# Kernel tuning notes

Hardware: AMD Instinct MI355X
Metric: run time of the kernel (lower is better)

## Reference

```python
import jax, jax.numpy as jnp
import numpy as np

B, N, DEG = 16, 2048, 16          # graphs, nodes per graph, avg out-degree
C_IN, HID, K = 64, 128, 32        # in_channels, hidden_channels, out_channels (clusters)
NT = B * N                        # total nodes
E = NT * DEG                      # total edges
GN_EPS = 1e-5


def setup_inputs() -> dict:
    key = jax.random.key(0)
    ks = jax.random.split(key, 6)
    x = jax.random.normal(ks[0], (NT, C_IN), jnp.float32)
    # within-graph random edges (sorted batch => node i belongs to graph i // N)
    src_l = jax.random.randint(ks[1], (E,), 0, N)
    dst_l = jax.random.randint(ks[2], (E,), 0, N)
    gid = jnp.repeat(jnp.arange(B, dtype=jnp.int32), N * DEG)
    edge_index = jnp.stack([gid * N + src_l, gid * N + dst_l]).astype(jnp.int32)
    batch = jnp.repeat(jnp.arange(B, dtype=jnp.int32), N)
    return dict(
        x=x, edge_index=edge_index, batch=batch,
        gn_weight=jnp.ones((C_IN,), jnp.float32),
        gn_bias=jnp.zeros((C_IN,), jnp.float32),
        gn_mean_scale=jnp.ones((C_IN,), jnp.float32),
        w1=jax.random.normal(ks[3], (C_IN, HID), jnp.float32) / np.float32(np.sqrt(C_IN)),
        b1=jnp.zeros((HID,), jnp.float32),
        w2=jax.random.normal(ks[4], (HID, K), jnp.float32) / np.float32(np.sqrt(HID)),
        b2=jnp.zeros((K,), jnp.float32),
    )


def reference(x, gn_weight, gn_bias, gn_mean_scale, w1, b1, w2, b2, edge_index, batch):
    # ---- GraphNorm (per-graph mean/var with learnable mean scale) ----
    ones_n = jnp.ones((NT,), x.dtype)
    cnt = jax.ops.segment_sum(ones_n, batch, num_segments=B)[:, None]        # [B,1]
    mean = jax.ops.segment_sum(x, batch, num_segments=B) / cnt              # [B,C]
    xm = x - gn_mean_scale * mean[batch]
    var = jax.ops.segment_sum(xm * xm, batch, num_segments=B) / cnt         # [B,C]
    h = gn_weight * xm / jnp.sqrt(var + GN_EPS)[batch] + gn_bias            # [NT,C_IN]

    # ---- GCNConv (add self-loops, symmetric D^-1/2 (A+I) D^-1/2) ----
    src, dst = edge_index[0], edge_index[1]
    loop = jnp.arange(NT, dtype=src.dtype)
    src_l = jnp.concatenate([src, loop])
    dst_l = jnp.concatenate([dst, loop])
    deg = jax.ops.segment_sum(jnp.ones_like(src_l, x.dtype), dst_l, num_segments=NT)
    dinv = jnp.where(deg > 0, jax.lax.rsqrt(deg), 0.0)
    norm = dinv[src_l] * dinv[dst_l]                                        # [E+NT]
    hw = h @ w1                                                             # [NT,HID]
    h = jax.ops.segment_sum(norm[:, None] * hw[src_l], dst_l, num_segments=NT) + b1
    h = jax.nn.selu(h)

    # ---- to_dense_batch / to_dense_adj (uniform graph sizes -> mask all True) ----
    xd = h.reshape(B, N, HID)                                               # [B,N,F]
    adj = jnp.zeros((B, N, N), x.dtype).at[batch[src], src % N, dst % N].add(1.0)

    # ---- DMoNPooling ----
    s = jax.nn.softmax(xd @ w2 + b2, axis=-1)                               # [B,N,K]
    out = jax.nn.selu(jnp.einsum('bnk,bnf->bkf', s, xd))                    # [B,K,F]
    sta = jnp.einsum('bnk,bnm->bkm', s, adj)                                # [B,K,N]
    out_adj = jnp.einsum('bkm,bml->bkl', sta, s)                            # [B,K,K]

    degrees = adj.sum(-1)                                                   # [B,N]
    m = degrees.sum(-1) / 2                                                 # [B]
    ca = jnp.einsum('bnk,bn->bk', s, degrees)                               # [B,K]
    normalizer = ca[:, :, None] * ca[:, None, :] / 2 / m[:, None, None]
    spectral_loss = (-jnp.einsum('bkk->b', out_adj - normalizer) / (2 * m)).mean()

    ss = jnp.einsum('bnk,bnl->bkl', s, s)                                   # [B,K,K]
    ss_fro = jnp.sqrt(jnp.sum(ss * ss, axis=(-2, -1), keepdims=True))
    eye = jnp.eye(K, dtype=x.dtype)
    diff = ss / ss_fro - eye / jnp.sqrt(jnp.float32(K))
    ortho_loss = jnp.sqrt(jnp.sum(diff * diff, axis=(-2, -1))).mean()

    cluster_size = s.sum(1)                                                 # [B,K]
    cluster_loss = (jnp.linalg.norm(cluster_size, axis=1) / N
                    * jnp.sqrt(jnp.float32(K)) - 1).mean()
    # (coarsened-adj renormalization in DMoNPooling is unused by Net's outputs)

    return jax.nn.log_softmax(out, axis=-1), spectral_loss + ortho_loss + cluster_loss, s
```

## Files before the change

### kernel.cpp

```cpp
#include <hip/hip_runtime.h>
#include <cmath>

static constexpr int B_  = 16;
static constexpr int N_  = 2048;
static constexpr int NT_ = 32768;
static constexpr int E_  = 524288;

static constexpr size_t OFF_HSC    = 0;
static constexpr size_t OFF_XD     = 2097152;
static constexpr size_t OFF_SWS    = 6291456;
static constexpr size_t OFF_PART   = 7340032;
static constexpr size_t OFF_DINV   = 9437184;
static constexpr size_t OFF_GSP    = 9469952;
static constexpr size_t OFF_GSP2   = 9478144;
static constexpr size_t OFF_SSP    = 9486336;
static constexpr size_t OFF_CAP    = 10010624;
static constexpr size_t OFF_CSP    = 10027008;
static constexpr size_t OFF_SPECP  = 10043392;
static constexpr size_t OFF_ICNTI  = 10043904;
static constexpr size_t OFF_ICNTO  = 10076672;
static constexpr size_t OFF_IROWS  = 10109440;
static constexpr size_t OFF_ICURS  = 10142212;
static constexpr size_t OFF_IESRC  = 10174980;

__device__ __forceinline__ float selu_f(float x) {
  return 1.0507009873554805f * (x > 0.f ? x : 1.6732632423543772f * expm1f(x));
}

__device__ __forceinline__ float block_sum_bcast(float v, float* sm) {
  int lane = threadIdx.x & 63, w = threadIdx.x >> 6;
#pragma unroll
  for (int off = 32; off; off >>= 1) v += __shfl_down(v, off);
  __syncthreads();
  if (lane == 0) sm[w] = v;
  __syncthreads();
  return sm[0] + sm[1] + sm[2] + sm[3];
}

__global__ __launch_bounds__(1024) void k_count(const int* ei, const float* x,
                                                int* cin, int* cout_,
                                                float* gsp, float* gsp2) {
  __shared__ int hin[2048], hout[2048];
  __shared__ float l1[16][64], l2[16][64];
  int blk = blockIdx.x;
  int tid = threadIdx.x;
  if (blk < 128) {
    int g = blk >> 3, j = blk & 7;
    int nbase = g * 2048, ebase = g * 32768 + j * 4096;
    hin[tid] = 0; hin[tid + 1024] = 0;
    hout[tid] = 0; hout[tid + 1024] = 0;
    __syncthreads();
#pragma unroll
    for (int it = 0; it < 4; it++) {
      int e = ebase + it * 1024 + tid;
      int s = ei[e], d = ei[E_ + e];
      atomicAdd(&hout[s - nbase], 1);
      atomicAdd(&hin[d - nbase], 1);
    }
    __syncthreads();
    atomicAdd(&cin[nbase + tid], hin[tid]);
    atomicAdd(&cin[nbase + tid + 1024], hin[tid + 1024]);
    atomicAdd(&cout_[nbase + tid], hout[tid]);
    atomicAdd(&cout_[nbase + tid + 1024], hout[tid + 1024]);
  } else {
    int gi = blk - 128;
    int b = gi >> 3, chunk = gi & 7;
    int c = tid & 63, r = tid >> 6;
    float s = 0.f, s2 = 0.f;
    const float* xb = x + ((size_t)b * N_ + (size_t)chunk * 256) * 64;
    for (int n = r; n < 256; n += 16) {
      float v = xb[n * 64 + c];
      s += v; s2 += v * v;
    }
    l1[r][c] = s; l2[r][c] = s2;
    __syncthreads();
    if (r == 0) {
      float t1 = 0.f, t2 = 0.f;
#pragma unroll
      for (int i = 0; i < 16; i++) { t1 += l1[i][c]; t2 += l2[i][c]; }
      gsp[gi * 64 + c] = t1;
      gsp2[gi * 64 + c] = t2;
    }
  }
}

__global__ __launch_bounds__(1024) void k_scan(const int* cin, int* rows, int* curs,
                                               float* dinv) {
  __shared__ int sb[1024];
  int g = blockIdx.x, tid = threadIdx.x;
  int nbase = g * 2048, ebase = g * 32768;
  int a = cin[nbase + 2 * tid], b2 = cin[nbase + 2 * tid + 1];
  sb[tid] = a + b2;
  __syncthreads();
  for (int off = 1; off < 1024; off <<= 1) {
    int add = (tid >= off) ? sb[tid - off] : 0;
    __syncthreads();
    sb[tid] += add;
    __syncthreads();
  }
  int pref = (tid > 0) ? sb[tid - 1] : 0;
  int r0 = ebase + pref, r1 = r0 + a;
  int n0 = nbase + 2 * tid;
  rows[n0] = r0; rows[n0 + 1] = r1;
  curs[n0] = r0; curs[n0 + 1] = r1;
  dinv[n0] = rsqrtf((float)(a + 1));
  dinv[n0 + 1] = rsqrtf((float)(b2 + 1));
  if (g == 15 && tid == 1023) rows[NT_] = E_;
}

__global__ void k_prep(const float* x, const float* gsp, const float* gsp2,
                       const float* gw, const float* gb, const float* gms,
                       const float* dinv, float* hsc,
                       const int* ei, int* curs, int* esrc) {
  __shared__ float shs[64], scs[64];
  int tid = threadIdx.x;
  int bgr = blockIdx.x >> 7;
  if (tid < 64) {
    float s = 0.f, s2 = 0.f;
#pragma unroll
    for (int c8 = 0; c8 < 8; c8++) {
      s  += gsp[(bgr * 8 + c8) * 64 + tid];
      s2 += gsp2[(bgr * 8 + c8) * 64 + tid];
    }
    float mean = s * (1.f / 2048.f);
    float a = gms[tid];
    float var = s2 * (1.f / 2048.f) - (2.f * a - a * a) * mean * mean;
    shs[tid] = a * mean;
    scs[tid] = gw[tid] * rsqrtf(var + 1e-5f);
  }
  __syncthreads();
  int idx = blockIdx.x * 256 + tid;
  int node = idx >> 4, g4 = (idx & 15) * 4;
  float di = dinv[node];
  float4 xv = *(const float4*)&x[(size_t)node * 64 + g4];
  float4 bb = *(const float4*)&gb[g4];
  float4 o;
  o.x = ((xv.x - shs[g4])     * scs[g4]     + bb.x) * di;
  o.y = ((xv.y - shs[g4 + 1]) * scs[g4 + 1] + bb.y) * di;
  o.z = ((xv.z - shs[g4 + 2]) * scs[g4 + 2] + bb.z) * di;
  o.w = ((xv.w - shs[g4 + 3]) * scs[g4 + 3] + bb.w) * di;
  *(float4*)&hsc[(size_t)node * 64 + g4] = o;
  int s = ei[idx], d = ei[E_ + idx];
  int pos = atomicAdd(&curs[d], 1);
  esrc[pos] = s;
}

__global__ __launch_bounds__(256) void k_mm1(const float* hsc, const float* dinv,
                                             const int* rows, const int* esrc,
                                             const float* w1, const float* b1,
                                             float* xd) {
  __shared__ float at[32 * 65];
  int tid = threadIdx.x;
  int n0 = blockIdx.x * 32;
  int wv = tid >> 6, c = tid & 63;
  for (int i = 0; i < 8; i++) {
    int nn = i * 4 + wv;
    int node = n0 + nn;
    int e0 = rows[node], e1 = rows[node + 1];
    float dd = dinv[node];
    float acc = hsc[(size_t)node * 64 + c];
    for (int e = e0; e < e1; e += 8) {
      int sidx[8]; float wt[8], hv[8];
#pragma unroll
      for (int j = 0; j < 8; j++) {
        int ee = e + j;
        sidx[j] = esrc[ee < e1 ? ee : e0];
        wt[j] = (ee < e1) ? 1.f : 0.f;
      }
#pragma unroll
      for (int j = 0; j < 8; j++) hv[j] = hsc[(size_t)sidx[j] * 64 + c];
#pragma unroll
      for (int j = 0; j < 8; j++) acc += wt[j] * hv[j];
    }
    at[nn * 65 + c] = dd * acc;
  }
  __syncthreads();
  int tx = tid & 31, ty = tid >> 5;
  int f0 = tx * 4, nn = ty * 4;
  float acc[4][4] = {};
  for (int k = 0; k < 64; k++) {
    float4 wvv = *(const float4*)&w1[k * 128 + f0];
#pragma unroll
    for (int i = 0; i < 4; i++) {
      float av = at[(nn + i) * 65 + k];
      acc[i][0] += av * wvv.x; acc[i][1] += av * wvv.y;
      acc[i][2] += av * wvv.z; acc[i][3] += av * wvv.w;
    }
  }
  float4 bv = *(const float4*)&b1[f0];
#pragma unroll
  for (int i = 0; i < 4; i++) {
    float4 o;
    o.x = selu_f(acc[i][0] + bv.x);
    o.y = selu_f(acc[i][1] + bv.y);
    o.z = selu_f(acc[i][2] + bv.z);
    o.w = selu_f(acc[i][3] + bv.w);
    *(float4*)&xd[(size_t)(n0 + nn + i) * 128 + f0] = o;
  }
}

__global__ __launch_bounds__(256) void k_mm2f(const float* xd, const float* w2,
                                              const float* b2, const int* cout_,
                                              float* s_ws, float* outs, float* ssp,
                                              float* cap, float* csp, float* part) {
  __shared__ float xt[64 * 129];
  __shared__ float w2s[128 * 32];
  __shared__ float st[64 * 33];
  __shared__ float r1[8][32], r2[8][32];
  int tid = threadIdx.x;
  int blk = blockIdx.x;
  int n0 = blk * 64;
  for (int i = tid; i < 4096; i += 256) w2s[i] = w2[i];
  for (int i = tid; i < 2048; i += 256) {
    int n = i >> 5, j4 = (i & 31) * 4;
    float4 v = *(const float4*)&xd[(size_t)(n0 + n) * 128 + j4];
    xt[n * 129 + j4] = v.x; xt[n * 129 + j4 + 1] = v.y;
    xt[n * 129 + j4 + 2] = v.z; xt[n * 129 + j4 + 3] = v.w;
  }
  __syncthreads();
  int ty = tid >> 3;
  int k0 = (tid & 7) * 4;
  float acc2[2][4] = {};
  for (int j = 0; j < 128; j++) {
    float4 wv = *(float4*)&w2s[j * 32 + k0];
    float x0 = xt[(ty * 2) * 129 + j];
    float x1 = xt[(ty * 2 + 1) * 129 + j];
    acc2[0][0] += x0 * wv.x; acc2[0][1] += x0 * wv.y; acc2[0][2] += x0 * wv.z; acc2[0][3] += x0 * wv.w;
    acc2[1][0] += x1 * wv.x; acc2[1][1] += x1 * wv.y; acc2[1][2] += x1 * wv.z; acc2[1][3] += x1 * wv.w;
  }
  float4 bv2 = *(const float4*)&b2[k0];
#pragma unroll
  for (int i = 0; i < 2; i++) {
    int n = ty * 2 + i;
    st[n * 33 + k0]     = acc2[i][0] + bv2.x;
    st[n * 33 + k0 + 1] = acc2[i][1] + bv2.y;
    st[n * 33 + k0 + 2] = acc2[i][2] + bv2.z;
    st[n * 33 + k0 + 3] = acc2[i][3] + bv2.w;
  }
  __syncthreads();
  if (tid < 64) {
    float m = -3.4e38f;
    for (int kk = 0; kk < 32; kk++) m = fmaxf(m, st[tid * 33 + kk]);
    float ssum = 0.f;
    for (int kk = 0; kk < 32; kk++) {
      float e = expf(st[tid * 33 + kk] - m);
      st[tid * 33 + kk] = e; ssum += e;
    }
    float inv = 1.f / ssum;
    for (int kk = 0; kk < 32; kk++) st[tid * 33 + kk] *= inv;
  }
  __syncthreads();
  for (int i = tid; i < 512; i += 256) {
    int n = i >> 3, q = (i & 7) * 4;
    float4 o = {st[n * 33 + q], st[n * 33 + q + 1], st[n * 33 + q + 2], st[n * 33 + q + 3]};
    *(float4*)&s_ws[(size_t)(n0 + n) * 32 + q] = o;
    float* op = &outs[(size_t)(n0 + n) * 32 + q];
    op[0] = o.x; op[1] = o.y; op[2] = o.z; op[3] = o.w;
  }
  {
    int k = tid >> 3, l0 = (tid & 7) * 4;
    float a0 = 0, a1 = 0, a2 = 0, a3 = 0;
    for (int n = 0; n < 64; n++) {
      float sk = st[n * 33 + k];
      a0 += sk * st[n * 33 + l0];     a1 += sk * st[n * 33 + l0 + 1];
      a2 += sk * st[n * 33 + l0 + 2]; a3 += sk * st[n * 33 + l0 + 3];
    }
    float4 o = {a0, a1, a2, a3};
    *(float4*)&ssp[(size_t)blk * 1024 + k * 32 + l0] = o;
  }
  {
    int k2 = tid & 31, r = tid >> 5;
    float aca = 0.f, acs = 0.f;
    for (int i = 0; i < 8; i++) {
      int n = i * 8 + r;
      float dg = (float)cout_[n0 + n];
      float v = st[n * 33 + k2];
      acs += v; aca += v * dg;
    }
    r1[r][k2] = aca; r2[r][k2] = acs;
    __syncthreads();
    if (r == 0) {
      float sa = 0.f, sc = 0.f;
#pragma unroll
      for (int i = 0; i < 8; i++) { sa += r1[i][k2]; sc += r2[i][k2]; }
      cap[blk * 32 + k2] = sa;
      csp[blk * 32 + k2] = sc;
    }
  }
  {
    int tx = tid & 31, ty2 = tid >> 5;
    int f0 = tx * 4, kk0 = ty2 * 4;
    float acc[4][4] = {};
    for (int n = 0; n < 64; n++) {
      float s0 = st[n * 33 + kk0], s1 = st[n * 33 + kk0 + 1];
      float s2 = st[n * 33 + kk0 + 2], s3 = st[n * 33 + kk0 + 3];
      float4 xv = {xt[n * 129 + f0], xt[n * 129 + f0 + 1], xt[n * 129 + f0 + 2], xt[n * 129 + f0 + 3]};
      acc[0][0] += s0 * xv.x; acc[0][1] += s0 * xv.y; acc[0][2] += s0 * xv.z; acc[0][3] += s0 * xv.w;
      acc[1][0] += s1 * xv.x; acc[1][1] += s1 * xv.y; acc[1][2] += s1 * xv.z; acc[1][3] += s1 * xv.w;
      acc[2][0] += s2 * xv.x; acc[2][1] += s2 * xv.y; acc[2][2] += s2 * xv.z; acc[2][3] += s2 * xv.w;
      acc[3][0] += s3 * xv.x; acc[3][1] += s3 * xv.y; acc[3][2] += s3 * xv.z; acc[3][3] += s3 * xv.w;
    }
#pragma unroll
    for (int i = 0; i < 4; i++) {
      float4 o = {acc[i][0], acc[i][1], acc[i][2], acc[i][3]};
      *(float4*)&part[(size_t)(blk * 32 + kk0 + i) * 128 + f0] = o;
    }
  }
}

__global__ __launch_bounds__(256) void k_spec(const int* ei, const float* s_ws,
                                              float* specp, float* lossp) {
  __shared__ float sm4[4];
  int blk = blockIdx.x, tid = threadIdx.x;
  if (blk == 0 && tid == 0) lossp[0] = 0.f;
  int ebase = blk * 1024;
  float acc = 0.f;
#pragma unroll
  for (int j = 0; j < 4; j++) {
    int e = ebase + j * 256 + tid;
    int s = ei[e], d = ei[E_ + e];
    const float4* ap = (const float4*)&s_ws[(size_t)s * 32];
    const float4* cp = (const float4*)&s_ws[(size_t)d * 32];
#pragma unroll
    for (int q = 0; q < 8; q++) {
      float4 u = ap[q], v = cp[q];
      acc += u.x * v.x + u.y * v.y + u.z * v.z + u.w * v.w;
    }
  }
  int lane = tid & 63, w = tid >> 6;
#pragma unroll
  for (int off = 32; off; off >>= 1) acc += __shfl_down(acc, off);
  if (lane == 0) sm4[w] = acc;
  __syncthreads();
  if (tid == 0) specp[blk] = sm4[0] + sm4[1] + sm4[2] + sm4[3];
}

__global__ void k_outf(const float* part, float* out0) {
  int row = blockIdx.x;
  int b = row >> 5, k = row & 31;
  int f = threadIdx.x;
  float v = 0.f;
#pragma unroll
  for (int c = 0; c < 32; c++) v += part[(size_t)((b * 32 + c) * 32 + k) * 128 + f];
  v = selu_f(v);
  int lane = threadIdx.x & 63, w = threadIdx.x >> 6;
  __shared__ float s1[2], s2[2];
  float m = v;
#pragma unroll
  for (int off = 32; off; off >>= 1) m = fmaxf(m, __shfl_down(m, off));
  if (lane == 0) s1[w] = m;
  __syncthreads();
  m = fmaxf(s1[0], s1[1]);
  float e = expf(v - m), t = e;
#pragma unroll
  for (int off = 32; off; off >>= 1) t += __shfl_down(t, off);
  if (lane == 0) s2[w] = t;
  __syncthreads();
  float tot = s2[0] + s2[1];
  out0[(size_t)row * 128 + f] = v - m - logf(tot);
}

__global__ void k_loss(const float* ssp, const float* csp, const float* cap,
                       const float* specp, float* loss) {
  int b = blockIdx.x;
  __shared__ float sm[4];
  int tid = threadIdx.x;
  float v0 = 0, v1 = 0, v2 = 0, v3 = 0;
  for (int c = 0; c < 32; c++) {
    float4 u = *(const float4*)&ssp[(size_t)(b * 32 + c) * 1024 + tid * 4];
    v0 += u.x; v1 += u.y; v2 += u.z; v3 += u.w;
  }
  float ssq = v0 * v0 + v1 * v1 + v2 * v2 + v3 * v3;
  ssq = block_sum_bcast(ssq, sm);
  float inv = 1.f / sqrtf(ssq);
  float dsq = 0.f;
  {
    int i0 = tid * 4;
    float vv[4] = {v0, v1, v2, v3};
#pragma unroll
    for (int j = 0; j < 4; j++) {
      int i = i0 + j;
      float d = vv[j] * inv;
      if ((i >> 5) == (i & 31)) d -= 0.17677669529663687f;
      dsq += d * d;
    }
  }
  dsq = block_sum_bcast(dsq, sm);
  float csq = 0.f, casq = 0.f;
  if (tid < 32) {
    float c1 = 0.f, c2 = 0.f;
    for (int c = 0; c < 32; c++) {
      c1 += csp[(size_t)(b * 32 + c) * 32 + tid];
      c2 += cap[(size_t)(b * 32 + c) * 32 + tid];
    }
    csq = c1 * c1; casq = c2 * c2;
  }
  csq = block_sum_bcast(csq, sm);
  casq = block_sum_bcast(casq, sm);
  float spec_sum = (tid < 32) ? specp[b * 32 + tid] : 0.f;
  spec_sum = block_sum_bcast(spec_sum, sm);
  if (tid == 0) {
    float ortho = sqrtf(dsq);
    float cl = sqrtf(csq) * (1.f / 2048.f) * 5.656854249492381f - 1.f;
    float m = 16384.f;
    float spec = -(spec_sum - casq / (2.f * m)) / (2.f * m);
    atomicAdd(loss, (spec + ortho + cl) * (1.f / 16.f));
  }
}

extern "C" void kernel_launch(void* const* d_in, const int* in_sizes, int n_in,
                              void* d_out, int out_size, void* d_ws, size_t ws_size,
                              hipStream_t stream) {
  (void)in_sizes; (void)n_in; (void)out_size; (void)ws_size;
  const float* x   = (const float*)d_in[0];
  const int*   ei  = (const int*)d_in[1];
  const float* gw  = (const float*)d_in[3];
  const float* gb  = (const float*)d_in[4];
  const float* gms = (const float*)d_in[5];
  const float* w1  = (const float*)d_in[6];
  const float* b1  = (const float*)d_in[7];
  const float* w2  = (const float*)d_in[8];
  const float* b2  = (const float*)d_in[9];
  float* out = (float*)d_out;
  float* ws  = (float*)d_ws;

  float* hsc    = ws + OFF_HSC;
  float* xd     = ws + OFF_XD;
  float* s_ws   = ws + OFF_SWS;
  float* part   = ws + OFF_PART;
  float* dinv   = ws + OFF_DINV;
  float* gsp    = ws + OFF_GSP;
  float* gsp2   = ws + OFF_GSP2;
  float* ssp    = ws + OFF_SSP;
  float* cap    = ws + OFF_CAP;
  float* csp    = ws + OFF_CSP;
  float* specp  = ws + OFF_SPECP;
  int*   cin    = (int*)(ws + OFF_ICNTI);
  int*   cout_  = (int*)(ws + OFF_ICNTO);
  int*   rows   = (int*)(ws + OFF_IROWS);
  int*   curs   = (int*)(ws + OFF_ICURS);
  int*   esrc   = (int*)(ws + OFF_IESRC);

  float* out0  = out;
  float* lossp = out + 65536;
  float* outs  = out + 65537;

  hipMemsetAsync((void*)cin, 0, 2 * NT_ * sizeof(int), stream);
  hipLaunchKernelGGL(k_count, dim3(256), dim3(1024), 0, stream, ei, x, cin, cout_, gsp, gsp2);
  hipLaunchKernelGGL(k_scan, dim3(16), dim3(1024), 0, stream, cin, rows, curs, dinv);
  hipLaunchKernelGGL(k_prep, dim3(2048), dim3(256), 0, stream,
                     x, gsp, gsp2, gw, gb, gms, dinv, hsc, ei, curs, esrc);
  hipLaunchKernelGGL(k_mm1, dim3(1024), dim3(256), 0, stream, hsc, dinv, rows, esrc, w1, b1, xd);
  hipLaunchKernelGGL(k_mm2f, dim3(512), dim3(256), 0, stream,
                     xd, w2, b2, cout_, s_ws, outs, ssp, cap, csp, part);
  hipLaunchKernelGGL(k_spec, dim3(512), dim3(256), 0, stream, ei, s_ws, specp, lossp);
  hipLaunchKernelGGL(k_outf, dim3(512), dim3(128), 0, stream, part, out0);
  hipLaunchKernelGGL(k_loss, dim3(16), dim3(256), 0, stream, ssp, csp, cap, specp, lossp);
}
```

Measured before the change: 208.0 us.

## Replace CSR build with per-block destination-filtered shared-memory aggregation; merge final kernels

Removes the prefix-scan kernel and the global-atomic bucketing of edges into CSR order. Each block instead streams all edges of its graph, uses a wave ballot to pick the edges whose destination falls in its 128-node slice, and accumulates neighbour features into shared memory with atomics before the W1 matmul. Degree normalisation is now computed on the fly from the in-degree counts. The log-softmax output kernel and the loss kernel are also merged into one launch. The cost is that every graph's edge list is read 16 times and the gather becomes a serial loop over matched lanes.

```diff
diff --git a/kernel.cpp b/kernel.cpp
--- a/kernel.cpp
+++ b/kernel.cpp
@@ -10,18 +10,14 @@
 static constexpr size_t OFF_XD     = 2097152;
 static constexpr size_t OFF_SWS    = 6291456;
 static constexpr size_t OFF_PART   = 7340032;
-static constexpr size_t OFF_DINV   = 9437184;
-static constexpr size_t OFF_GSP    = 9469952;
-static constexpr size_t OFF_GSP2   = 9478144;
-static constexpr size_t OFF_SSP    = 9486336;
-static constexpr size_t OFF_CAP    = 10010624;
-static constexpr size_t OFF_CSP    = 10027008;
-static constexpr size_t OFF_SPECP  = 10043392;
-static constexpr size_t OFF_ICNTI  = 10043904;
-static constexpr size_t OFF_ICNTO  = 10076672;
-static constexpr size_t OFF_IROWS  = 10109440;
-static constexpr size_t OFF_ICURS  = 10142212;
-static constexpr size_t OFF_IESRC  = 10174980;
+static constexpr size_t OFF_GSP    = 9437184;
+static constexpr size_t OFF_GSP2   = 9445376;
+static constexpr size_t OFF_SSP    = 9453568;
+static constexpr size_t OFF_CAP    = 9977856;
+static constexpr size_t OFF_CSP    = 9994240;
+static constexpr size_t OFF_SPECP  = 10010624;
+static constexpr size_t OFF_ICNTI  = 10011136;
+static constexpr size_t OFF_ICNTO  = 10043904;
 
 __device__ __forceinline__ float selu_f(float x) {
   return 1.0507009873554805f * (x > 0.f ? x : 1.6732632423543772f * expm1f(x));
@@ -84,34 +80,9 @@
   }
 }
 
-__global__ __launch_bounds__(1024) void k_scan(const int* cin, int* rows, int* curs,
-                                               float* dinv) {
-  __shared__ int sb[1024];
-  int g = blockIdx.x, tid = threadIdx.x;
-  int nbase = g * 2048, ebase = g * 32768;
-  int a = cin[nbase + 2 * tid], b2 = cin[nbase + 2 * tid + 1];
-  sb[tid] = a + b2;
-  __syncthreads();
-  for (int off = 1; off < 1024; off <<= 1) {
-    int add = (tid >= off) ? sb[tid - off] : 0;
-    __syncthreads();
-    sb[tid] += add;
-    __syncthreads();
-  }
-  int pref = (tid > 0) ? sb[tid - 1] : 0;
-  int r0 = ebase + pref, r1 = r0 + a;
-  int n0 = nbase + 2 * tid;
-  rows[n0] = r0; rows[n0 + 1] = r1;
-  curs[n0] = r0; curs[n0 + 1] = r1;
-  dinv[n0] = rsqrtf((float)(a + 1));
-  dinv[n0 + 1] = rsqrtf((float)(b2 + 1));
-  if (g == 15 && tid == 1023) rows[NT_] = E_;
-}
-
 __global__ void k_prep(const float* x, const float* gsp, const float* gsp2,
                        const float* gw, const float* gb, const float* gms,
-                       const float* dinv, float* hsc,
-                       const int* ei, int* curs, int* esrc) {
+                       const int* cin, float* hsc) {
   __shared__ float shs[64], scs[64];
   int tid = threadIdx.x;
   int bgr = blockIdx.x >> 7;
@@ -131,7 +102,7 @@
   __syncthreads();
   int idx = blockIdx.x * 256 + tid;
   int node = idx >> 4, g4 = (idx & 15) * 4;
-  float di = dinv[node];
+  float di = rsqrtf((float)(cin[node] + 1));
   float4 xv = *(const float4*)&x[(size_t)node * 64 + g4];
   float4 bb = *(const float4*)&gb[g4];
   float4 o;
@@ -140,62 +111,64 @@
   o.z = ((xv.z - shs[g4 + 2]) * scs[g4 + 2] + bb.z) * di;
   o.w = ((xv.w - shs[g4 + 3]) * scs[g4 + 3] + bb.w) * di;
   *(float4*)&hsc[(size_t)node * 64 + g4] = o;
-  int s = ei[idx], d = ei[E_ + idx];
-  int pos = atomicAdd(&curs[d], 1);
-  esrc[pos] = s;
-}
-
-__global__ __launch_bounds__(256) void k_mm1(const float* hsc, const float* dinv,
-                                             const int* rows, const int* esrc,
-                                             const float* w1, const float* b1,
-                                             float* xd) {
-  __shared__ float at[32 * 65];
+}
+
+__global__ __launch_bounds__(1024) void k_aggmm(const int* ei, const float* hsc,
+                                                const int* cin, const float* w1,
+                                                const float* b1, float* xd) {
+  __shared__ float acc[128 * 65];
+  int blk = blockIdx.x;
+  int g = blk >> 4, j = blk & 15;
+  int nbase = g * 2048, dstLo = j * 128;
+  int ebase = g * 32768;
   int tid = threadIdx.x;
-  int n0 = blockIdx.x * 32;
-  int wv = tid >> 6, c = tid & 63;
-  for (int i = 0; i < 8; i++) {
-    int nn = i * 4 + wv;
-    int node = n0 + nn;
-    int e0 = rows[node], e1 = rows[node + 1];
-    float dd = dinv[node];
-    float acc = hsc[(size_t)node * 64 + c];
-    for (int e = e0; e < e1; e += 8) {
-      int sidx[8]; float wt[8], hv[8];
-#pragma unroll
-      for (int j = 0; j < 8; j++) {
-        int ee = e + j;
-        sidx[j] = esrc[ee < e1 ? ee : e0];
-        wt[j] = (ee < e1) ? 1.f : 0.f;
-      }
-#pragma unroll
-      for (int j = 0; j < 8; j++) hv[j] = hsc[(size_t)sidx[j] * 64 + c];
-#pragma unroll
-      for (int j = 0; j < 8; j++) acc += wt[j] * hv[j];
-    }
-    at[nn * 65 + c] = dd * acc;
+  int wave = tid >> 6, lane = tid & 63;
+  for (int i = tid; i < 8320; i += 1024) acc[i] = 0.f;
+  __syncthreads();
+  int wbase = ebase + wave * 2048;
+  for (int it = 0; it < 32; it++) {
+    int e = wbase + it * 64 + lane;
+    int s = ei[e];
+    int d = ei[E_ + e];
+    int loc = d - nbase - dstLo;
+    unsigned long long mask = __ballot((unsigned)loc < 128u);
+    while (mask) {
+      int b = __ffsll((unsigned long long)mask) - 1;
+      mask &= mask - 1;
+      int sb = __shfl(s, b);
+      int lb = __shfl(loc, b);
+      atomicAdd(&acc[lb * 65 + lane], hsc[(size_t)sb * 64 + lane]);
+    }
+  }
+  __syncthreads();
+  for (int i = tid; i < 8192; i += 1024) {
+    int n = i >> 6, c = i & 63;
+    int node = nbase + dstLo + n;
+    float dd = rsqrtf((float)(cin[node] + 1));
+    acc[n * 65 + c] = dd * (acc[n * 65 + c] + hsc[(size_t)node * 64 + c]);
   }
   __syncthreads();
   int tx = tid & 31, ty = tid >> 5;
   int f0 = tx * 4, nn = ty * 4;
-  float acc[4][4] = {};
+  float a4[4][4] = {};
   for (int k = 0; k < 64; k++) {
-    float4 wvv = *(const float4*)&w1[k * 128 + f0];
+    float4 wv = *(const float4*)&w1[k * 128 + f0];
 #pragma unroll
     for (int i = 0; i < 4; i++) {
-      float av = at[(nn + i) * 65 + k];
-      acc[i][0] += av * wvv.x; acc[i][1] += av * wvv.y;
-      acc[i][2] += av * wvv.z; acc[i][3] += av * wvv.w;
+      float av = acc[(nn + i) * 65 + k];
+      a4[i][0] += av * wv.x; a4[i][1] += av * wv.y;
+      a4[i][2] += av * wv.z; a4[i][3] += av * wv.w;
     }
   }
   float4 bv = *(const float4*)&b1[f0];
 #pragma unroll
   for (int i = 0; i < 4; i++) {
     float4 o;
-    o.x = selu_f(acc[i][0] + bv.x);
-    o.y = selu_f(acc[i][1] + bv.y);
-    o.z = selu_f(acc[i][2] + bv.z);
-    o.w = selu_f(acc[i][3] + bv.w);
-    *(float4*)&xd[(size_t)(n0 + nn + i) * 128 + f0] = o;
+    o.x = selu_f(a4[i][0] + bv.x);
+    o.y = selu_f(a4[i][1] + bv.y);
+    o.z = selu_f(a4[i][2] + bv.z);
+    o.w = selu_f(a4[i][3] + bv.w);
+    *(float4*)&xd[(size_t)(nbase + dstLo + nn + i) * 128 + f0] = o;
   }
 }
 
@@ -335,76 +308,81 @@
   if (tid == 0) specp[blk] = sm4[0] + sm4[1] + sm4[2] + sm4[3];
 }
 
-__global__ void k_outf(const float* part, float* out0) {
-  int row = blockIdx.x;
-  int b = row >> 5, k = row & 31;
-  int f = threadIdx.x;
-  float v = 0.f;
-#pragma unroll
-  for (int c = 0; c < 32; c++) v += part[(size_t)((b * 32 + c) * 32 + k) * 128 + f];
-  v = selu_f(v);
-  int lane = threadIdx.x & 63, w = threadIdx.x >> 6;
-  __shared__ float s1[2], s2[2];
-  float m = v;
-#pragma unroll
-  for (int off = 32; off; off >>= 1) m = fmaxf(m, __shfl_down(m, off));
-  if (lane == 0) s1[w] = m;
-  __syncthreads();
-  m = fmaxf(s1[0], s1[1]);
-  float e = expf(v - m), t = e;
-#pragma unroll
-  for (int off = 32; off; off >>= 1) t += __shfl_down(t, off);
-  if (lane == 0) s2[w] = t;
-  __syncthreads();
-  float tot = s2[0] + s2[1];
-  out0[(size_t)row * 128 + f] = v - m - logf(tot);
-}
-
-__global__ void k_loss(const float* ssp, const float* csp, const float* cap,
-                       const float* specp, float* loss) {
-  int b = blockIdx.x;
-  __shared__ float sm[4];
+__global__ __launch_bounds__(256) void k_fin2(const float* part, const float* ssp,
+                                              const float* csp, const float* cap,
+                                              const float* specp, float* out0,
+                                              float* loss) {
+  __shared__ float sred[4];
+  int blk = blockIdx.x;
   int tid = threadIdx.x;
-  float v0 = 0, v1 = 0, v2 = 0, v3 = 0;
-  for (int c = 0; c < 32; c++) {
-    float4 u = *(const float4*)&ssp[(size_t)(b * 32 + c) * 1024 + tid * 4];
-    v0 += u.x; v1 += u.y; v2 += u.z; v3 += u.w;
-  }
-  float ssq = v0 * v0 + v1 * v1 + v2 * v2 + v3 * v3;
-  ssq = block_sum_bcast(ssq, sm);
-  float inv = 1.f / sqrtf(ssq);
-  float dsq = 0.f;
-  {
-    int i0 = tid * 4;
-    float vv[4] = {v0, v1, v2, v3};
-#pragma unroll
-    for (int j = 0; j < 4; j++) {
-      int i = i0 + j;
-      float d = vv[j] * inv;
-      if ((i >> 5) == (i & 31)) d -= 0.17677669529663687f;
-      dsq += d * d;
-    }
-  }
-  dsq = block_sum_bcast(dsq, sm);
-  float csq = 0.f, casq = 0.f;
-  if (tid < 32) {
-    float c1 = 0.f, c2 = 0.f;
+  if (blk < 256) {
+    int half = tid >> 7;
+    int f = tid & 127;
+    int row = blk * 2 + half;
+    int b = row >> 5, k = row & 31;
+    float v = 0.f;
+#pragma unroll
+    for (int c = 0; c < 32; c++) v += part[(size_t)((b * 32 + c) * 32 + k) * 128 + f];
+    v = selu_f(v);
+    int lane = tid & 63, w = tid >> 6;
+    float m = v;
+#pragma unroll
+    for (int off = 32; off; off >>= 1) m = fmaxf(m, __shfl_down(m, off));
+    if (lane == 0) sred[w] = m;
+    __syncthreads();
+    m = fmaxf(sred[half * 2], sred[half * 2 + 1]);
+    float e = expf(v - m);
+    float t = e;
+    __syncthreads();
+#pragma unroll
+    for (int off = 32; off; off >>= 1) t += __shfl_down(t, off);
+    if (lane == 0) sred[w] = t;
+    __syncthreads();
+    float tot = sred[half * 2] + sred[half * 2 + 1];
+    out0[(size_t)row * 128 + f] = v - m - logf(tot);
+  } else {
+    int b = blk - 256;
+    float v0 = 0, v1 = 0, v2 = 0, v3 = 0;
     for (int c = 0; c < 32; c++) {
-      c1 += csp[(size_t)(b * 32 + c) * 32 + tid];
-      c2 += cap[(size_t)(b * 32 + c) * 32 + tid];
-    }
-    csq = c1 * c1; casq = c2 * c2;
-  }
-  csq = block_sum_bcast(csq, sm);
-  casq = block_sum_bcast(casq, sm);
-  float spec_sum = (tid < 32) ? specp[b * 32 + tid] : 0.f;
-  spec_sum = block_sum_bcast(spec_sum, sm);
-  if (tid == 0) {
-    float ortho = sqrtf(dsq);
-    float cl = sqrtf(csq) * (1.f / 2048.f) * 5.656854249492381f - 1.f;
-    float m = 16384.f;
-    float spec = -(spec_sum - casq / (2.f * m)) / (2.f * m);
-    atomicAdd(loss, (spec + ortho + cl) * (1.f / 16.f));
+      float4 u = *(const float4*)&ssp[(size_t)(b * 32 + c) * 1024 + tid * 4];
+      v0 += u.x; v1 += u.y; v2 += u.z; v3 += u.w;
+    }
+    float ssq = v0 * v0 + v1 * v1 + v2 * v2 + v3 * v3;
+    ssq = block_sum_bcast(ssq, sred);
+    float inv = 1.f / sqrtf(ssq);
+    float dsq = 0.f;
+    {
+      int i0 = tid * 4;
+      float vv[4] = {v0, v1, v2, v3};
+#pragma unroll
+      for (int jj = 0; jj < 4; jj++) {
+        int i = i0 + jj;
+        float d = vv[jj] * inv;
+        if ((i >> 5) == (i & 31)) d -= 0.17677669529663687f;
+        dsq += d * d;
+      }
+    }
+    dsq = block_sum_bcast(dsq, sred);
+    float csq = 0.f, casq = 0.f;
+    if (tid < 32) {
+      float c1 = 0.f, c2 = 0.f;
+      for (int c = 0; c < 32; c++) {
+        c1 += csp[(size_t)(b * 32 + c) * 32 + tid];
+        c2 += cap[(size_t)(b * 32 + c) * 32 + tid];
+      }
+      csq = c1 * c1; casq = c2 * c2;
+    }
+    csq = block_sum_bcast(csq, sred);
+    casq = block_sum_bcast(casq, sred);
+    float spec_sum = (tid < 32) ? specp[b * 32 + tid] : 0.f;
+    spec_sum = block_sum_bcast(spec_sum, sred);
+    if (tid == 0) {
+      float ortho = sqrtf(dsq);
+      float cl = sqrtf(csq) * (1.f / 2048.f) * 5.656854249492381f - 1.f;
+      float m = 16384.f;
+      float spec = -(spec_sum - casq / (2.f * m)) / (2.f * m);
+      atomicAdd(loss, (spec + ortho + cl) * (1.f / 16.f));
+    }
   }
 }
 
@@ -428,7 +406,6 @@
   float* xd     = ws + OFF_XD;
   float* s_ws   = ws + OFF_SWS;
   float* part   = ws + OFF_PART;
-  float* dinv   = ws + OFF_DINV;
   float* gsp    = ws + OFF_GSP;
   float* gsp2   = ws + OFF_GSP2;
   float* ssp    = ws + OFF_SSP;
@@ -437,9 +414,6 @@
   float* specp  = ws + OFF_SPECP;
   int*   cin    = (int*)(ws + OFF_ICNTI);
   int*   cout_  = (int*)(ws + OFF_ICNTO);
-  int*   rows   = (int*)(ws + OFF_IROWS);
-  int*   curs   = (int*)(ws + OFF_ICURS);
-  int*   esrc   = (int*)(ws + OFF_IESRC);
 
   float* out0  = out;
   float* lossp = out + 65536;
@@ -447,13 +421,12 @@
 
   hipMemsetAsync((void*)cin, 0, 2 * NT_ * sizeof(int), stream);
   hipLaunchKernelGGL(k_count, dim3(256), dim3(1024), 0, stream, ei, x, cin, cout_, gsp, gsp2);
-  hipLaunchKernelGGL(k_scan, dim3(16), dim3(1024), 0, stream, cin, rows, curs, dinv);
   hipLaunchKernelGGL(k_prep, dim3(2048), dim3(256), 0, stream,
-                     x, gsp, gsp2, gw, gb, gms, dinv, hsc, ei, curs, esrc);
-  hipLaunchKernelGGL(k_mm1, dim3(1024), dim3(256), 0, stream, hsc, dinv, rows, esrc, w1, b1, xd);
+                     x, gsp, gsp2, gw, gb, gms, cin, hsc);
+  hipLaunchKernelGGL(k_aggmm, dim3(256), dim3(1024), 0, stream, ei, hsc, cin, w1, b1, xd);
   hipLaunchKernelGGL(k_mm2f, dim3(512), dim3(256), 0, stream,
                      xd, w2, b2, cout_, s_ws, outs, ssp, cap, csp, part);
   hipLaunchKernelGGL(k_spec, dim3(512), dim3(256), 0, stream, ei, s_ws, specp, lossp);
-  hipLaunchKernelGGL(k_outf, dim3(512), dim3(128), 0, stream, part, out0);
-  hipLaunchKernelGGL(k_loss, dim3(16), dim3(256), 0, stream, ssp, csp, cap, specp, lossp);
-}
+  hipLaunchKernelGGL(k_fin2, dim3(272), dim3(256), 0, stream,
+                     part, ssp, csp, cap, specp, out0, lossp);
+}
```

Measured after the change: 359.4 us. 1.73x slower.

## Replace global atomic CSR build with per-block histograms and shared-memory scatter

Applied to the files above, without the earlier changes.

The edge-count kernel now writes per-block in/out histograms instead of doing global atomics, so the memset is no longer needed. The scan kernel sums these histograms and emits a per-block starting cursor. The CSR scatter then runs with shared-memory atomics in dedicated blocks alongside the GraphNorm prep. The output softmax and loss kernels are merged into one launch. This removes global atomic contention and two launches, at the cost of extra histogram traffic.

```diff
diff --git a/kernel.cpp b/kernel.cpp
--- a/kernel.cpp
+++ b/kernel.cpp
@@ -10,18 +10,19 @@
 static constexpr size_t OFF_XD     = 2097152;
 static constexpr size_t OFF_SWS    = 6291456;
 static constexpr size_t OFF_PART   = 7340032;
-static constexpr size_t OFF_DINV   = 9437184;
-static constexpr size_t OFF_GSP    = 9469952;
-static constexpr size_t OFF_GSP2   = 9478144;
-static constexpr size_t OFF_SSP    = 9486336;
-static constexpr size_t OFF_CAP    = 10010624;
-static constexpr size_t OFF_CSP    = 10027008;
-static constexpr size_t OFF_SPECP  = 10043392;
-static constexpr size_t OFF_ICNTI  = 10043904;
-static constexpr size_t OFF_ICNTO  = 10076672;
-static constexpr size_t OFF_IROWS  = 10109440;
-static constexpr size_t OFF_ICURS  = 10142212;
-static constexpr size_t OFF_IESRC  = 10174980;
+static constexpr size_t OFF_GSP    = 9437184;
+static constexpr size_t OFF_GSP2   = 9445376;
+static constexpr size_t OFF_SSP    = 9453568;
+static constexpr size_t OFF_CAP    = 9977856;
+static constexpr size_t OFF_CSP    = 9994240;
+static constexpr size_t OFF_SPECP  = 10010624;
+static constexpr size_t OFF_DINV   = 10011136;
+static constexpr size_t OFF_IHIN   = 10043904;
+static constexpr size_t OFF_IHOUT  = 10306048;
+static constexpr size_t OFF_ICURS  = 10568192;
+static constexpr size_t OFF_IROWS  = 10830336;
+static constexpr size_t OFF_ICNTO  = 10863108;
+static constexpr size_t OFF_IESRC  = 10895876;
 
 __device__ __forceinline__ float selu_f(float x) {
   return 1.0507009873554805f * (x > 0.f ? x : 1.6732632423543772f * expm1f(x));
@@ -38,15 +39,15 @@
 }
 
 __global__ __launch_bounds__(1024) void k_count(const int* ei, const float* x,
-                                                int* cin, int* cout_,
+                                                int* histin, int* histout,
                                                 float* gsp, float* gsp2) {
   __shared__ int hin[2048], hout[2048];
   __shared__ float l1[16][64], l2[16][64];
   int blk = blockIdx.x;
   int tid = threadIdx.x;
   if (blk < 128) {
-    int g = blk >> 3, j = blk & 7;
-    int nbase = g * 2048, ebase = g * 32768 + j * 4096;
+    int g = blk >> 3, p = blk & 7;
+    int nbase = g * 2048, ebase = g * 32768 + p * 4096;
     hin[tid] = 0; hin[tid + 1024] = 0;
     hout[tid] = 0; hout[tid + 1024] = 0;
     __syncthreads();
@@ -58,10 +59,10 @@
       atomicAdd(&hin[d - nbase], 1);
     }
     __syncthreads();
-    atomicAdd(&cin[nbase + tid], hin[tid]);
-    atomicAdd(&cin[nbase + tid + 1024], hin[tid + 1024]);
-    atomicAdd(&cout_[nbase + tid], hout[tid]);
-    atomicAdd(&cout_[nbase + tid + 1024], hout[tid + 1024]);
+    histin[blk * 2048 + tid] = hin[tid];
+    histin[blk * 2048 + tid + 1024] = hin[tid + 1024];
+    histout[blk * 2048 + tid] = hout[tid];
+    histout[blk * 2048 + tid + 1024] = hout[tid + 1024];
   } else {
     int gi = blk - 128;
     int b = gi >> 3, chunk = gi & 7;
@@ -84,13 +85,24 @@
   }
 }
 
-__global__ __launch_bounds__(1024) void k_scan(const int* cin, int* rows, int* curs,
+__global__ __launch_bounds__(1024) void k_scan(const int* histin, const int* histout,
+                                               int* rows, int* cursp, int* cout_,
                                                float* dinv) {
   __shared__ int sb[1024];
   int g = blockIdx.x, tid = threadIdx.x;
   int nbase = g * 2048, ebase = g * 32768;
-  int a = cin[nbase + 2 * tid], b2 = cin[nbase + 2 * tid + 1];
-  sb[tid] = a + b2;
+  int n0 = 2 * tid, n1 = 2 * tid + 1;
+  int h0[8], h1[8];
+  int a = 0, b = 0, o0 = 0, o1 = 0;
+#pragma unroll
+  for (int p = 0; p < 8; p++) {
+    h0[p] = histin[(g * 8 + p) * 2048 + n0];
+    h1[p] = histin[(g * 8 + p) * 2048 + n1];
+    a += h0[p]; b += h1[p];
+    o0 += histout[(g * 8 + p) * 2048 + n0];
+    o1 += histout[(g * 8 + p) * 2048 + n1];
+  }
+  sb[tid] = a + b;
   __syncthreads();
   for (int off = 1; off < 1024; off <<= 1) {
     int add = (tid >= off) ? sb[tid - off] : 0;
@@ -100,49 +112,73 @@
   }
   int pref = (tid > 0) ? sb[tid - 1] : 0;
   int r0 = ebase + pref, r1 = r0 + a;
-  int n0 = nbase + 2 * tid;
-  rows[n0] = r0; rows[n0 + 1] = r1;
-  curs[n0] = r0; curs[n0 + 1] = r1;
-  dinv[n0] = rsqrtf((float)(a + 1));
-  dinv[n0 + 1] = rsqrtf((float)(b2 + 1));
+  rows[nbase + n0] = r0;
+  rows[nbase + n1] = r1;
+  dinv[nbase + n0] = rsqrtf((float)(a + 1));
+  dinv[nbase + n1] = rsqrtf((float)(b + 1));
+  cout_[nbase + n0] = o0;
+  cout_[nbase + n1] = o1;
+  int run0 = r0, run1 = r1;
+#pragma unroll
+  for (int p = 0; p < 8; p++) {
+    cursp[(g * 8 + p) * 2048 + n0] = run0; run0 += h0[p];
+    cursp[(g * 8 + p) * 2048 + n1] = run1; run1 += h1[p];
+  }
   if (g == 15 && tid == 1023) rows[NT_] = E_;
 }
 
-__global__ void k_prep(const float* x, const float* gsp, const float* gsp2,
-                       const float* gw, const float* gb, const float* gms,
-                       const float* dinv, float* hsc,
-                       const int* ei, int* curs, int* esrc) {
+__global__ __launch_bounds__(256) void k_prepb(const float* x, const float* gsp,
+                                               const float* gsp2, const float* gw,
+                                               const float* gb, const float* gms,
+                                               const float* dinv, float* hsc,
+                                               const int* ei, const int* cursp,
+                                               int* esrc) {
   __shared__ float shs[64], scs[64];
+  __shared__ int cur[2048];
   int tid = threadIdx.x;
-  int bgr = blockIdx.x >> 7;
-  if (tid < 64) {
-    float s = 0.f, s2 = 0.f;
-#pragma unroll
-    for (int c8 = 0; c8 < 8; c8++) {
-      s  += gsp[(bgr * 8 + c8) * 64 + tid];
-      s2 += gsp2[(bgr * 8 + c8) * 64 + tid];
-    }
-    float mean = s * (1.f / 2048.f);
-    float a = gms[tid];
-    float var = s2 * (1.f / 2048.f) - (2.f * a - a * a) * mean * mean;
-    shs[tid] = a * mean;
-    scs[tid] = gw[tid] * rsqrtf(var + 1e-5f);
-  }
-  __syncthreads();
-  int idx = blockIdx.x * 256 + tid;
-  int node = idx >> 4, g4 = (idx & 15) * 4;
-  float di = dinv[node];
-  float4 xv = *(const float4*)&x[(size_t)node * 64 + g4];
-  float4 bb = *(const float4*)&gb[g4];
-  float4 o;
-  o.x = ((xv.x - shs[g4])     * scs[g4]     + bb.x) * di;
-  o.y = ((xv.y - shs[g4 + 1]) * scs[g4 + 1] + bb.y) * di;
-  o.z = ((xv.z - shs[g4 + 2]) * scs[g4 + 2] + bb.z) * di;
-  o.w = ((xv.w - shs[g4 + 3]) * scs[g4 + 3] + bb.w) * di;
-  *(float4*)&hsc[(size_t)node * 64 + g4] = o;
-  int s = ei[idx], d = ei[E_ + idx];
-  int pos = atomicAdd(&curs[d], 1);
-  esrc[pos] = s;
+  int blk = blockIdx.x;
+  if (blk < 2048) {
+    int bgr = blk >> 7;
+    if (tid < 64) {
+      float s = 0.f, s2 = 0.f;
+#pragma unroll
+      for (int c8 = 0; c8 < 8; c8++) {
+        s  += gsp[(bgr * 8 + c8) * 64 + tid];
+        s2 += gsp2[(bgr * 8 + c8) * 64 + tid];
+      }
+      float mean = s * (1.f / 2048.f);
+      float a = gms[tid];
+      float var = s2 * (1.f / 2048.f) - (2.f * a - a * a) * mean * mean;
+      shs[tid] = a * mean;
+      scs[tid] = gw[tid] * rsqrtf(var + 1e-5f);
+    }
+    __syncthreads();
+    int idx = blk * 256 + tid;
+    int node = idx >> 4, g4 = (idx & 15) * 4;
+    float di = dinv[node];
+    float4 xv = *(const float4*)&x[(size_t)node * 64 + g4];
+    float4 bb = *(const float4*)&gb[g4];
+    float4 o;
+    o.x = ((xv.x - shs[g4])     * scs[g4]     + bb.x) * di;
+    o.y = ((xv.y - shs[g4 + 1]) * scs[g4 + 1] + bb.y) * di;
+    o.z = ((xv.z - shs[g4 + 2]) * scs[g4 + 2] + bb.z) * di;
+    o.w = ((xv.w - shs[g4 + 3]) * scs[g4 + 3] + bb.w) * di;
+    *(float4*)&hsc[(size_t)node * 64 + g4] = o;
+  } else {
+    int bb = blk - 2048;
+    int g = bb >> 3, p = bb & 7;
+    int nbase = g * 2048;
+    int ebase = g * 32768 + p * 4096;
+    for (int i = tid; i < 2048; i += 256) cur[i] = cursp[bb * 2048 + i];
+    __syncthreads();
+#pragma unroll
+    for (int it = 0; it < 16; it++) {
+      int e = ebase + it * 256 + tid;
+      int s = ei[e], d = ei[E_ + e];
+      int pos = atomicAdd(&cur[d - nbase], 1);
+      esrc[pos] = s;
+    }
+  }
 }
 
 __global__ __launch_bounds__(256) void k_mm1(const float* hsc, const float* dinv,
@@ -335,76 +371,81 @@
   if (tid == 0) specp[blk] = sm4[0] + sm4[1] + sm4[2] + sm4[3];
 }
 
-__global__ void k_outf(const float* part, float* out0) {
-  int row = blockIdx.x;
-  int b = row >> 5, k = row & 31;
-  int f = threadIdx.x;
-  float v = 0.f;
-#pragma unroll
-  for (int c = 0; c < 32; c++) v += part[(size_t)((b * 32 + c) * 32 + k) * 128 + f];
-  v = selu_f(v);
-  int lane = threadIdx.x & 63, w = threadIdx.x >> 6;
-  __shared__ float s1[2], s2[2];
-  float m = v;
-#pragma unroll
-  for (int off = 32; off; off >>= 1) m = fmaxf(m, __shfl_down(m, off));
-  if (lane == 0) s1[w] = m;
-  __syncthreads();
-  m = fmaxf(s1[0], s1[1]);
-  float e = expf(v - m), t = e;
-#pragma unroll
-  for (int off = 32; off; off >>= 1) t += __shfl_down(t, off);
-  if (lane == 0) s2[w] = t;
-  __syncthreads();
-  float tot = s2[0] + s2[1];
-  out0[(size_t)row * 128 + f] = v - m - logf(tot);
-}
-
-__global__ void k_loss(const float* ssp, const float* csp, const float* cap,
-                       const float* specp, float* loss) {
-  int b = blockIdx.x;
-  __shared__ float sm[4];
+__global__ __launch_bounds__(256) void k_fin2(const float* part, const float* ssp,
+                                              const float* csp, const float* cap,
+                                              const float* specp, float* out0,
+                                              float* loss) {
+  __shared__ float sred[4];
+  int blk = blockIdx.x;
   int tid = threadIdx.x;
-  float v0 = 0, v1 = 0, v2 = 0, v3 = 0;
-  for (int c = 0; c < 32; c++) {
-    float4 u = *(const float4*)&ssp[(size_t)(b * 32 + c) * 1024 + tid * 4];
-    v0 += u.x; v1 += u.y; v2 += u.z; v3 += u.w;
-  }
-  float ssq = v0 * v0 + v1 * v1 + v2 * v2 + v3 * v3;
-  ssq = block_sum_bcast(ssq, sm);
-  float inv = 1.f / sqrtf(ssq);
-  float dsq = 0.f;
-  {
-    int i0 = tid * 4;
-    float vv[4] = {v0, v1, v2, v3};
-#pragma unroll
-    for (int j = 0; j < 4; j++) {
-      int i = i0 + j;
-      float d = vv[j] * inv;
-      if ((i >> 5) == (i & 31)) d -= 0.17677669529663687f;
-      dsq += d * d;
-    }
-  }
-  dsq = block_sum_bcast(dsq, sm);
-  float csq = 0.f, casq = 0.f;
-  if (tid < 32) {
-    float c1 = 0.f, c2 = 0.f;
+  if (blk < 256) {
+    int half = tid >> 7;
+    int f = tid & 127;
+    int row = blk * 2 + half;
+    int b = row >> 5, k = row & 31;
+    float v = 0.f;
+#pragma unroll
+    for (int c = 0; c < 32; c++) v += part[(size_t)((b * 32 + c) * 32 + k) * 128 + f];
+    v = selu_f(v);
+    int lane = tid & 63, w = tid >> 6;
+    float m = v;
+#pragma unroll
+    for (int off = 32; off; off >>= 1) m = fmaxf(m, __shfl_down(m, off));
+    if (lane == 0) sred[w] = m;
+    __syncthreads();
+    m = fmaxf(sred[half * 2], sred[half * 2 + 1]);
+    float e = expf(v - m);
+    float t = e;
+    __syncthreads();
+#pragma unroll
+    for (int off = 32; off; off >>= 1) t += __shfl_down(t, off);
+    if (lane == 0) sred[w] = t;
+    __syncthreads();
+    float tot = sred[half * 2] + sred[half * 2 + 1];
+    out0[(size_t)row * 128 + f] = v - m - logf(tot);
+  } else {
+    int b = blk - 256;
+    float v0 = 0, v1 = 0, v2 = 0, v3 = 0;
     for (int c = 0; c < 32; c++) {
-      c1 += csp[(size_t)(b * 32 + c) * 32 + tid];
-      c2 += cap[(size_t)(b * 32 + c) * 32 + tid];
-    }
-    csq = c1 * c1; casq = c2 * c2;
-  }
-  csq = block_sum_bcast(csq, sm);
-  casq = block_sum_bcast(casq, sm);
-  float spec_sum = (tid < 32) ? specp[b * 32 + tid] : 0.f;
-  spec_sum = block_sum_bcast(spec_sum, sm);
-  if (tid == 0) {
-    float ortho = sqrtf(dsq);
-    float cl = sqrtf(csq) * (1.f / 2048.f) * 5.656854249492381f - 1.f;
-    float m = 16384.f;
-    float spec = -(spec_sum - casq / (2.f * m)) / (2.f * m);
-    atomicAdd(loss, (spec + ortho + cl) * (1.f / 16.f));
+      float4 u = *(const float4*)&ssp[(size_t)(b * 32 + c) * 1024 + tid * 4];
+      v0 += u.x; v1 += u.y; v2 += u.z; v3 += u.w;
+    }
+    float ssq = v0 * v0 + v1 * v1 + v2 * v2 + v3 * v3;
+    ssq = block_sum_bcast(ssq, sred);
+    float inv = 1.f / sqrtf(ssq);
+    float dsq = 0.f;
+    {
+      int i0 = tid * 4;
+      float vv[4] = {v0, v1, v2, v3};
+#pragma unroll
+      for (int jj = 0; jj < 4; jj++) {
+        int i = i0 + jj;
+        float d = vv[jj] * inv;
+        if ((i >> 5) == (i & 31)) d -= 0.17677669529663687f;
+        dsq += d * d;
+      }
+    }
+    dsq = block_sum_bcast(dsq, sred);
+    float csq = 0.f, casq = 0.f;
+    if (tid < 32) {
+      float c1 = 0.f, c2 = 0.f;
+      for (int c = 0; c < 32; c++) {
+        c1 += csp[(size_t)(b * 32 + c) * 32 + tid];
+        c2 += cap[(size_t)(b * 32 + c) * 32 + tid];
+      }
+      csq = c1 * c1; casq = c2 * c2;
+    }
+    csq = block_sum_bcast(csq, sred);
+    casq = block_sum_bcast(casq, sred);
+    float spec_sum = (tid < 32) ? specp[b * 32 + tid] : 0.f;
+    spec_sum = block_sum_bcast(spec_sum, sred);
+    if (tid == 0) {
+      float ortho = sqrtf(dsq);
+      float cl = sqrtf(csq) * (1.f / 2048.f) * 5.656854249492381f - 1.f;
+      float m = 16384.f;
+      float spec = -(spec_sum - casq / (2.f * m)) / (2.f * m);
+      atomicAdd(loss, (spec + ortho + cl) * (1.f / 16.f));
+    }
   }
 }
 
@@ -428,32 +469,33 @@
   float* xd     = ws + OFF_XD;
   float* s_ws   = ws + OFF_SWS;
   float* part   = ws + OFF_PART;
-  float* dinv   = ws + OFF_DINV;
   float* gsp    = ws + OFF_GSP;
   float* gsp2   = ws + OFF_GSP2;
   float* ssp    = ws + OFF_SSP;
   float* cap    = ws + OFF_CAP;
   float* csp    = ws + OFF_CSP;
   float* specp  = ws + OFF_SPECP;
-  int*   cin    = (int*)(ws + OFF_ICNTI);
+  float* dinv   = ws + OFF_DINV;
+  int*   histin = (int*)(ws + OFF_IHIN);
+  int*   histout= (int*)(ws + OFF_IHOUT);
+  int*   cursp  = (int*)(ws + OFF_ICURS);
+  int*   rows   = (int*)(ws + OFF_IROWS);
   int*   cout_  = (int*)(ws + OFF_ICNTO);
-  int*   rows   = (int*)(ws + OFF_IROWS);
-  int*   curs   = (int*)(ws + OFF_ICURS);
   int*   esrc   = (int*)(ws + OFF_IESRC);
 
   float* out0  = out;
   float* lossp = out + 65536;
   float* outs  = out + 65537;
 
-  hipMemsetAsync((void*)cin, 0, 2 * NT_ * sizeof(int), stream);
-  hipLaunchKernelGGL(k_count, dim3(256), dim3(1024), 0, stream, ei, x, cin, cout_, gsp, gsp2);
-  hipLaunchKernelGGL(k_scan, dim3(16), dim3(1024), 0, stream, cin, rows, curs, dinv);
-  hipLaunchKernelGGL(k_prep, dim3(2048), dim3(256), 0, stream,
-                     x, gsp, gsp2, gw, gb, gms, dinv, hsc, ei, curs, esrc);
+  hipLaunchKernelGGL(k_count, dim3(256), dim3(1024), 0, stream, ei, x, histin, histout, gsp, gsp2);
+  hipLaunchKernelGGL(k_scan, dim3(16), dim3(1024), 0, stream,
+                     histin, histout, rows, cursp, cout_, dinv);
+  hipLaunchKernelGGL(k_prepb, dim3(2176), dim3(256), 0, stream,
+                     x, gsp, gsp2, gw, gb, gms, dinv, hsc, ei, cursp, esrc);
   hipLaunchKernelGGL(k_mm1, dim3(1024), dim3(256), 0, stream, hsc, dinv, rows, esrc, w1, b1, xd);
   hipLaunchKernelGGL(k_mm2f, dim3(512), dim3(256), 0, stream,
                      xd, w2, b2, cout_, s_ws, outs, ssp, cap, csp, part);
   hipLaunchKernelGGL(k_spec, dim3(512), dim3(256), 0, stream, ei, s_ws, specp, lossp);
-  hipLaunchKernelGGL(k_outf, dim3(512), dim3(128), 0, stream, part, out0);
-  hipLaunchKernelGGL(k_loss, dim3(16), dim3(256), 0, stream, ssp, csp, cap, specp, lossp);
-}
+  hipLaunchKernelGGL(k_fin2, dim3(272), dim3(256), 0, stream,
+                     part, ssp, csp, cap, specp, out0, lossp);
+}
```

Measured after the change: 202.5 us. 1.03x faster.
